# Performance work log

Measured on AMD Instinct MI355X. Metric: run time of the kernel, lower is better.

## Reference

```python
import jax, jax.numpy as jnp
import numpy as np

B, F_DIM, C = 256, 512, 100000
M_MARGIN, S_SCALE, K_VP = 0.4, 64.0, 0.7


def l2norm(x, eps):
    n = jnp.linalg.norm(x, axis=-1, keepdims=True)
    return x / jnp.maximum(n, eps)


def setup_inputs() -> dict:
    key = jax.random.key(0)
    k1, k2, k3, k4 = jax.random.split(key, 4)
    inp = jax.random.normal(k1, (B, F_DIM), dtype=jnp.float32)
    # kaiming_normal_(a=1, fan_in, leaky_relu): std = sqrt(2/(1+a^2))/sqrt(fan_in) = 1/sqrt(F)
    weight = jax.random.normal(k2, (C, F_DIM), dtype=jnp.float32) / np.sqrt(F_DIM)
    queue = jax.random.normal(k3, (C, F_DIM), dtype=jnp.float32)
    label = jax.random.randint(k4, (B,), 0, C, dtype=jnp.int32)
    return {"input": inp, "weight": weight, "queue": queue, "label": label, "epoch": 5}


def reference(input, weight, queue, label, epoch):
    emb = l2norm(input, 1e-5)                              # [B, F]
    cos_theta = emb @ l2norm(weight, 1e-5).T               # [B, C]
    one_hot = jax.nn.one_hot(label, C, dtype=cos_theta.dtype)
    cosine = cos_theta - M_MARGIN * one_hot

    # update_virtual_prototype (detached): diag(queue[labels] @ emb.T) == rowwise dot
    emb_d = jax.lax.stop_gradient(emb)
    q_rows = queue[label]                                  # [B, F]
    drift = jnp.sum(q_rows * emb_d, axis=-1)               # [B]
    factor = jax.nn.soft_sign(drift)[:, None]              # softsign update criteria
    new_rows = l2norm(factor * q_rows + (1.0 - factor) * emb_d, 1e-12)
    queue_upd = queue.at[label].set(new_rows)

    # epoch + 1 >= start_vp_epoch (4): virtual-prototype branch
    vp_sim = emb @ jax.lax.stop_gradient(l2norm(queue_upd, 1e-12)).T   # [B, C]
    rows = jnp.arange(B)
    diag = vp_sim[rows, label]
    vp_sim = vp_sim.at[rows, label].set(diag - K_VP * jax.lax.stop_gradient(diag))

    cosine_full = jnp.concatenate([cosine, vp_sim], axis=0)           # [2B, C]
    labels_full = jnp.concatenate([one_hot, one_hot], axis=0)         # [2B, C]
    logits = S_SCALE * cosine_full

    # EPL loss
    sum_neg = jnp.sum((1.0 - labels_full) * jnp.exp(logits), axis=1)
    sum_pos = jnp.sum(labels_full * jnp.exp(-logits), axis=1)
    loss = jnp.log(1.0 + sum_neg * sum_pos)
    return jnp.mean(loss)
```

## Files before the change

### kernel.cpp

```cpp
#include <hip/hip_runtime.h>
#include <math.h>

#define B 256
#define F 512
#define C 100000
#define S_SCALE 64.0f
#define M_MARGIN 0.4f
#define K_VP 0.7f

#define BN 32
#define NTILES (C / BN)
#define NT_TOT (2 * NTILES)
#define NBLK 256

typedef __bf16 bf16x8 __attribute__((ext_vector_type(8)));
typedef float  floatx4 __attribute__((ext_vector_type(4)));

__global__ void embnew_kernel(const float* __restrict__ input, const float* __restrict__ queue,
                              const int* __restrict__ label,
                              __bf16* __restrict__ embb_sw, float* __restrict__ newrows) {
    int i = blockIdx.x;
    int t = threadIdx.x;
    const float* x = input + (size_t)i * F;
    float x0 = x[t], x1 = x[t + 256];
    float p = x0 * x0 + x1 * x1;
    __shared__ float red[4];
    for (int off = 32; off > 0; off >>= 1) p += __shfl_down(p, off, 64);
    if ((t & 63) == 0) red[t >> 6] = p;
    __syncthreads();
    float tot = red[0] + red[1] + red[2] + red[3];
    float inv = 1.0f / fmaxf(sqrtf(tot), 1e-5f);
    float e0 = x0 * inv, e1 = x1 * inv;
    {
        int R = i >> 4, ln = i & 15;
        int k = t;
        embb_sw[(size_t)(((R * 16 + (k >> 5)) * 64 + ln + 16 * ((k & 31) >> 3)) * 8 + (k & 7))] = (__bf16)e0;
        k = t + 256;
        embb_sw[(size_t)(((R * 16 + (k >> 5)) * 64 + ln + 16 * ((k & 31) >> 3)) * 8 + (k & 7))] = (__bf16)e1;
    }
    int l = label[i];
    const float* qr = queue + (size_t)l * F;
    float q0 = qr[t], q1 = qr[t + 256];
    float pd = q0 * e0 + q1 * e1;
    __syncthreads();
    for (int off = 32; off > 0; off >>= 1) pd += __shfl_down(pd, off, 64);
    if ((t & 63) == 0) red[t >> 6] = pd;
    __syncthreads();
    float drift = red[0] + red[1] + red[2] + red[3];
    float f = drift / (1.0f + fabsf(drift));
    float v0 = f * q0 + (1.0f - f) * e0;
    float v1 = f * q1 + (1.0f - f) * e1;
    float p2 = v0 * v0 + v1 * v1;
    __syncthreads();
    for (int off = 32; off > 0; off >>= 1) p2 += __shfl_down(p2, off, 64);
    if ((t & 63) == 0) red[t >> 6] = p2;
    __syncthreads();
    float tot2 = red[0] + red[1] + red[2] + red[3];
    float inv2 = 1.0f / fmaxf(sqrtf(tot2), 1e-12f);
    newrows[(size_t)i * F + t]       = v0 * inv2;
    newrows[(size_t)i * F + t + 256] = v1 * inv2;
}

__global__ void init_kernel(int* __restrict__ map) {
    int idx = blockIdx.x * 256 + threadIdx.x;
    if (idx < C) map[idx] = -1;
}

__global__ void scatter_kernel(const int* __restrict__ label, int* __restrict__ map) {
    atomicMax(&map[label[threadIdx.x]], (int)threadIdx.x);
}

__global__ __launch_bounds__(1024, 4) void gemm_epl_kernel(
        const __bf16* __restrict__ embb_sw,
        const float* __restrict__ weight,
        const float* __restrict__ queue,
        const float* __restrict__ newrows,
        const int* __restrict__ map,
        const int* __restrict__ label,
        float* __restrict__ partials,
        float* __restrict__ posvals) {
    int tid = threadIdx.x;
    int w = tid >> 6;
    int l = tid & 63;
    int ln = l & 15;
    int q = l >> 4;
    int ctS = w & 1;
    int ksA = w >> 1;
    int cl = ctS * 16 + ln;

    __shared__ __align__(16) __bf16 bS[32 * 512];
    __shared__ float colpart_s[32][33];
    __shared__ float colinv_s[32];
    __shared__ int label_s[B];

    if (tid < B) label_s[tid] = label[tid];

    bf16x8 aA[16];
#pragma unroll
    for (int ks = 0; ks < 16; ++ks)
        aA[ks] = *(const bf16x8*)(embb_sw + ((size_t)((w * 16 + ks) * 64 + l) << 3));

    int ft0 = (int)(((long)blockIdx.x * NT_TOT) / NBLK);
    int ft1 = (int)(((long)(blockIdx.x + 1) * NT_TOT) / NBLK);

    float4 u[4];
    float ns0[4] = {0.f, 0.f, 0.f, 0.f};
    float ns1[4] = {0.f, 0.f, 0.f, 0.f};

    auto issue_loads = [&](int ft) {
        int s1 = (ft >= NTILES);
        int tile = ft - s1 * NTILES;
        int c = tile * BN + cl;
        const float* bp;
        if (!s1) bp = weight + (size_t)c * F;
        else {
            int mi = map[c];
            bp = (mi >= 0) ? newrows + (size_t)mi * F : queue + (size_t)c * F;
        }
        int k0 = ksA * 32 + q * 8;
        u[0] = *(const float4*)(bp + k0);
        u[1] = *(const float4*)(bp + k0 + 4);
        u[2] = *(const float4*)(bp + k0 + 256);
        u[3] = *(const float4*)(bp + k0 + 260);
    };

    issue_loads(ft0);

    for (int ft = ft0; ft < ft1; ++ft) {
        int s1 = (ft >= NTILES);
        int tile = ft - s1 * NTILES;
        int cbase = tile * BN;

        {
            float4 u0 = u[0], u1 = u[1], u2 = u[2], u3 = u[3];
            float ss = u0.x * u0.x + u0.y * u0.y + u0.z * u0.z + u0.w * u0.w
                     + u1.x * u1.x + u1.y * u1.y + u1.z * u1.z + u1.w * u1.w
                     + u2.x * u2.x + u2.y * u2.y + u2.z * u2.z + u2.w * u2.w
                     + u3.x * u3.x + u3.y * u3.y + u3.z * u3.z + u3.w * u3.w;
            bf16x8 p0, p1;
            p0[0] = (__bf16)u0.x; p0[1] = (__bf16)u0.y; p0[2] = (__bf16)u0.z; p0[3] = (__bf16)u0.w;
            p0[4] = (__bf16)u1.x; p0[5] = (__bf16)u1.y; p0[6] = (__bf16)u1.z; p0[7] = (__bf16)u1.w;
            p1[0] = (__bf16)u2.x; p1[1] = (__bf16)u2.y; p1[2] = (__bf16)u2.z; p1[3] = (__bf16)u2.w;
            p1[4] = (__bf16)u3.x; p1[5] = (__bf16)u3.y; p1[6] = (__bf16)u3.z; p1[7] = (__bf16)u3.w;
            *(bf16x8*)&bS[(size_t)(((ksA * 2 + ctS) * 64 + l) * 8)]       = p0;
            *(bf16x8*)&bS[(size_t)((((ksA + 8) * 2 + ctS) * 64 + l) * 8)] = p1;
            colpart_s[cl][ksA * 4 + q] = ss;
        }
        __syncthreads();

        if (tid < 32) {
            float s = 0.f;
#pragma unroll
            for (int p = 0; p < 32; ++p) s += colpart_s[tid][p];
            colinv_s[tid] = 1.0f / fmaxf(sqrtf(s), s1 ? 1e-12f : 1e-5f);
        }

        if (ft + 1 < ft1) issue_loads(ft + 1);

        floatx4 acc0 = (floatx4){0.f, 0.f, 0.f, 0.f};
        floatx4 acc1 = (floatx4){0.f, 0.f, 0.f, 0.f};
#pragma unroll
        for (int ks = 0; ks < 16; ++ks) {
            bf16x8 b0 = *(const bf16x8*)&bS[(size_t)(((ks * 2 + 0) * 64 + l) * 8)];
            bf16x8 b1 = *(const bf16x8*)&bS[(size_t)(((ks * 2 + 1) * 64 + l) * 8)];
            acc0 = __builtin_amdgcn_mfma_f32_16x16x32_bf16(aA[ks], b0, acc0, 0, 0, 0);
            acc1 = __builtin_amdgcn_mfma_f32_16x16x32_bf16(aA[ks], b1, acc1, 0, 0, 0);
        }
        __syncthreads();

#define EPL_BODY(NS)                                                          \
        _Pragma("unroll")                                                     \
        for (int r = 0; r < 4; ++r) {                                         \
            int row = w * 16 + q * 4 + r;                                     \
            int lab = label_s[row];                                           \
            float v0 = acc0[r] * colinv_s[ln];                                \
            float v1 = acc1[r] * colinv_s[16 + ln];                           \
            if (cbase + ln == lab) posvals[s1 * B + row] = v0;                \
            else NS[r] += __expf(S_SCALE * v0);                               \
            if (cbase + 16 + ln == lab) posvals[s1 * B + row] = v1;           \
            else NS[r] += __expf(S_SCALE * v1);                               \
        }
        if (!s1) { EPL_BODY(ns0) } else { EPL_BODY(ns1) }
#undef EPL_BODY
    }

#pragma unroll
    for (int r = 0; r < 4; ++r) {
#pragma unroll
        for (int off = 1; off <= 8; off <<= 1) {
            ns0[r] += __shfl_xor(ns0[r], off, 64);
            ns1[r] += __shfl_xor(ns1[r], off, 64);
        }
    }
    if (ln == 0) {
        int rb = w * 16 + q * 4;
        float4 a = make_float4(ns0[0], ns0[1], ns0[2], ns0[3]);
        float4 b = make_float4(ns1[0], ns1[1], ns1[2], ns1[3]);
        *(float4*)&partials[(size_t)blockIdx.x * 512 + rb]       = a;
        *(float4*)&partials[(size_t)blockIdx.x * 512 + 256 + rb] = b;
    }
}

__global__ void reduce_kernel(const float* __restrict__ partials, float* __restrict__ negacc) {
    int j = blockIdx.x * 256 + threadIdx.x;
    float s = 0.f;
    for (int bx = 0; bx < NBLK; ++bx) s += partials[(size_t)bx * 512 + j];
    negacc[j] = s;
}

__global__ void loss_kernel(const float* __restrict__ negacc, const float* __restrict__ posvals,
                            float* __restrict__ out) {
    int t = threadIdx.x;
    float l1 = log1pf(negacc[t] * __expf(-S_SCALE * (posvals[t] - M_MARGIN)));
    float l2 = log1pf(negacc[B + t] * __expf(-S_SCALE * (1.0f - K_VP) * posvals[B + t]));
    float p = l1 + l2;
    __shared__ float red[4];
    for (int off = 32; off > 0; off >>= 1) p += __shfl_down(p, off, 64);
    if ((t & 63) == 0) red[t >> 6] = p;
    __syncthreads();
    if (t == 0) out[0] = (red[0] + red[1] + red[2] + red[3]) / (2.0f * B);
}

extern "C" void kernel_launch(void* const* d_in, const int* in_sizes, int n_in,
                              void* d_out, int out_size, void* d_ws, size_t ws_size,
                              hipStream_t stream) {
    const float* input  = (const float*)d_in[0];
    const float* weight = (const float*)d_in[1];
    const float* queue  = (const float*)d_in[2];
    const int*   label  = (const int*)d_in[3];
    float* out = (float*)d_out;

    char* ws = (char*)d_ws;
    __bf16* embb_sw  = (__bf16*)(ws);
    float*  newrows  = (float*)(ws + (256 << 10));
    float*  negacc   = (float*)(ws + (768 << 10));
    float*  posvals  = (float*)(ws + (768 << 10) + 2048);
    int*    map      = (int*)  (ws + (768 << 10) + 4096);
    float*  partials = (float*)(ws + (1200 << 10));

    init_kernel<<<(C + 255) / 256, 256, 0, stream>>>(map);
    scatter_kernel<<<1, B, 0, stream>>>(label, map);
    embnew_kernel<<<B, 256, 0, stream>>>(input, queue, label, embb_sw, newrows);
    gemm_epl_kernel<<<NBLK, 1024, 0, stream>>>(embb_sw, weight, queue, newrows, map,
                                               label, partials, posvals);
    reduce_kernel<<<2, 256, 0, stream>>>(partials, negacc);
    loss_kernel<<<1, 256, 0, stream>>>(negacc, posvals, out);
}
```

Baseline: 434.3 us.

## Double GEMM grid, reload A fragments per tile, fuse reduce and loss kernels

```diff
diff --git a/kernel.cpp b/kernel.cpp
--- a/kernel.cpp
+++ b/kernel.cpp
@@ -11,7 +11,7 @@
 #define BN 32
 #define NTILES (C / BN)
 #define NT_TOT (2 * NTILES)
-#define NBLK 256
+#define NBLK 512
 
 typedef __bf16 bf16x8 __attribute__((ext_vector_type(8)));
 typedef float  floatx4 __attribute__((ext_vector_type(4)));
@@ -70,7 +70,7 @@
     atomicMax(&map[label[threadIdx.x]], (int)threadIdx.x);
 }
 
-__global__ __launch_bounds__(1024, 4) void gemm_epl_kernel(
+__global__ __launch_bounds__(1024, 8) void gemm_epl_kernel(
         const __bf16* __restrict__ embb_sw,
         const float* __restrict__ weight,
         const float* __restrict__ queue,
@@ -95,11 +95,6 @@
 
     if (tid < B) label_s[tid] = label[tid];
 
-    bf16x8 aA[16];
-#pragma unroll
-    for (int ks = 0; ks < 16; ++ks)
-        aA[ks] = *(const bf16x8*)(embb_sw + ((size_t)((w * 16 + ks) * 64 + l) << 3));
-
     int ft0 = (int)(((long)blockIdx.x * NT_TOT) / NBLK);
     int ft1 = (int)(((long)(blockIdx.x + 1) * NT_TOT) / NBLK);
 
@@ -161,10 +156,11 @@
         floatx4 acc1 = (floatx4){0.f, 0.f, 0.f, 0.f};
 #pragma unroll
         for (int ks = 0; ks < 16; ++ks) {
+            bf16x8 a = *(const bf16x8*)(embb_sw + ((size_t)((w * 16 + ks) * 64 + l) << 3));
             bf16x8 b0 = *(const bf16x8*)&bS[(size_t)(((ks * 2 + 0) * 64 + l) * 8)];
             bf16x8 b1 = *(const bf16x8*)&bS[(size_t)(((ks * 2 + 1) * 64 + l) * 8)];
-            acc0 = __builtin_amdgcn_mfma_f32_16x16x32_bf16(aA[ks], b0, acc0, 0, 0, 0);
-            acc1 = __builtin_amdgcn_mfma_f32_16x16x32_bf16(aA[ks], b1, acc1, 0, 0, 0);
+            acc0 = __builtin_amdgcn_mfma_f32_16x16x32_bf16(a, b0, acc0, 0, 0, 0);
+            acc1 = __builtin_amdgcn_mfma_f32_16x16x32_bf16(a, b1, acc1, 0, 0, 0);
         }
         __syncthreads();
 
@@ -201,24 +197,31 @@
     }
 }
 
-__global__ void reduce_kernel(const float* __restrict__ partials, float* __restrict__ negacc) {
-    int j = blockIdx.x * 256 + threadIdx.x;
+__global__ void finish_kernel(const float* __restrict__ partials,
+                              const float* __restrict__ posvals,
+                              float* __restrict__ out) {
+    int j = threadIdx.x;
     float s = 0.f;
     for (int bx = 0; bx < NBLK; ++bx) s += partials[(size_t)bx * 512 + j];
-    negacc[j] = s;
-}
-
-__global__ void loss_kernel(const float* __restrict__ negacc, const float* __restrict__ posvals,
-                            float* __restrict__ out) {
-    int t = threadIdx.x;
-    float l1 = log1pf(negacc[t] * __expf(-S_SCALE * (posvals[t] - M_MARGIN)));
-    float l2 = log1pf(negacc[B + t] * __expf(-S_SCALE * (1.0f - K_VP) * posvals[B + t]));
-    float p = l1 + l2;
-    __shared__ float red[4];
+    __shared__ float neg[512];
+    neg[j] = s;
+    __syncthreads();
+    float p = 0.f;
+    if (j < 256) {
+        float l1 = log1pf(neg[j]       * __expf(-S_SCALE * (posvals[j] - M_MARGIN)));
+        float l2 = log1pf(neg[256 + j] * __expf(-S_SCALE * (1.0f - K_VP) * posvals[256 + j]));
+        p = l1 + l2;
+    }
     for (int off = 32; off > 0; off >>= 1) p += __shfl_down(p, off, 64);
-    if ((t & 63) == 0) red[t >> 6] = p;
-    __syncthreads();
-    if (t == 0) out[0] = (red[0] + red[1] + red[2] + red[3]) / (2.0f * B);
+    __shared__ float red[8];
+    if ((j & 63) == 0) red[j >> 6] = p;
+    __syncthreads();
+    if (j == 0) {
+        float t = 0.f;
+#pragma unroll
+        for (int i = 0; i < 8; ++i) t += red[i];
+        out[0] = t / (2.0f * B);
+    }
 }
 
 extern "C" void kernel_launch(void* const* d_in, const int* in_sizes, int n_in,
@@ -233,7 +236,6 @@
     char* ws = (char*)d_ws;
     __bf16* embb_sw  = (__bf16*)(ws);
     float*  newrows  = (float*)(ws + (256 << 10));
-    float*  negacc   = (float*)(ws + (768 << 10));
     float*  posvals  = (float*)(ws + (768 << 10) + 2048);
     int*    map      = (int*)  (ws + (768 << 10) + 4096);
     float*  partials = (float*)(ws + (1200 << 10));
@@ -243,6 +245,5 @@
     embnew_kernel<<<B, 256, 0, stream>>>(input, queue, label, embb_sw, newrows);
     gemm_epl_kernel<<<NBLK, 1024, 0, stream>>>(embb_sw, weight, queue, newrows, map,
                                                label, partials, posvals);
-    reduce_kernel<<<2, 256, 0, stream>>>(partials, negacc);
-    loss_kernel<<<1, 256, 0, stream>>>(negacc, posvals, out);
-}
+    finish_kernel<<<1, 512, 0, stream>>>(partials, posvals, out);
+}
```

Result: slower. 635.4 us (+46.3%).
